# Performance work log

Hardware: AMD Instinct MI355X
Metric: run time of the kernel (lower is better)

## Reference

```python
import jax, jax.numpy as jnp
import numpy as np

B, L, D, H, DF = 8, 1024, 512, 8, 2048
NBLK = 3  # three TemporalAttentionBlocks


def _ln(x, g, b, eps=1e-5):
    m = x.mean(-1, keepdims=True)
    v = x.var(-1, keepdims=True)
    return (x - m) / jnp.sqrt(v + eps) * g + b


def setup_inputs() -> dict:
    key = jax.random.key(0)
    ks = iter(jax.random.split(key, 64))
    def w(i, o):
        return jax.random.normal(next(ks), (i, o), jnp.float32) * (1.0 / np.sqrt(i))
    def ws(n, i, o):
        return jax.random.normal(next(ks), (n, i, o), jnp.float32) * (1.0 / np.sqrt(i))
    return dict(
        x=jax.random.normal(next(ks), (B, L, D), jnp.float32),
        # outer multi-head attention (AttentionLayer) params
        aw_q=w(D, D), ab_q=jnp.zeros((D,), jnp.float32),
        aw_k=w(D, D), ab_k=jnp.zeros((D,), jnp.float32),
        aw_v=w(D, D), ab_v=jnp.zeros((D,), jnp.float32),
        aw_o=w(D, D), ab_o=jnp.zeros((D,), jnp.float32),
        n1g=jnp.ones((D,), jnp.float32), n1b=jnp.zeros((D,), jnp.float32),
        n2g=jnp.ones((D,), jnp.float32), n2b=jnp.zeros((D,), jnp.float32),
        # 3 stacked TemporalAttentionBlock params
        tqw=ws(NBLK, D, D), tqb=jnp.zeros((NBLK, D), jnp.float32),
        tkw=ws(NBLK, D, D), tkb=jnp.zeros((NBLK, D), jnp.float32),
        tvw=ws(NBLK, D, D), tvb=jnp.zeros((NBLK, D), jnp.float32),
        tow=ws(NBLK, D, D), tob=jnp.zeros((NBLK, D), jnp.float32),
        tf1w=ws(NBLK, D, DF), tf1b=jnp.zeros((NBLK, DF), jnp.float32),
        tf2w=ws(NBLK, DF, D), tf2b=jnp.zeros((NBLK, D), jnp.float32),
        tng=jnp.ones((NBLK, D), jnp.float32), tnb=jnp.zeros((NBLK, D), jnp.float32),
    )


def _temporal_block(x, qw, qb, kw, kb, vw, vb, ow, ob, f1w, f1b, f2w, f2b, ng, nb):
    b, l, d = x.shape
    q = x @ qw + qb
    k = x @ kw + kb
    v = x @ vw + vb
    # NOTE: no 1/sqrt(d) scaling, as in the original
    probs = jax.nn.softmax(jnp.einsum('bld,bsd->bls', q, k), axis=-1)
    out = jnp.einsum('bls,bsd->bld', probs, v)
    # faithful to original transpose(1,2).contiguous().view(-1, L, D): a
    # memory-reinterpreting reshape of [B,D,L] into [B,L,D]
    out = jnp.swapaxes(out, 1, 2).reshape(b, l, d)
    x = x + (out @ ow + ob)
    res = x
    xn = _ln(x, ng, nb)
    ff = jax.nn.relu(xn @ f1w + f1b) @ f2w + f2b
    return res + ff


def reference(x, aw_q, ab_q, aw_k, ab_k, aw_v, ab_v, aw_o, ab_o,
              n1g, n1b, n2g, n2b,
              tqw, tqb, tkw, tkb, tvw, tvb, tow, tob,
              tf1w, tf1b, tf2w, tf2b, tng, tnb):
    b, l, d = x.shape
    e = d // H
    q = (x @ aw_q + ab_q).reshape(b, l, H, e)
    k = (x @ aw_k + ab_k).reshape(b, l, H, e)
    v = (x @ aw_v + ab_v).reshape(b, l, H, e)
    A = jax.nn.softmax(jnp.einsum('blhe,bshe->bhls', q, k) / np.sqrt(e).astype(np.float32), axis=-1)
    new_x = jnp.einsum('bhls,bshe->blhe', A, v).reshape(b, l, d) @ aw_o + ab_o
    x = _ln(x + new_x, n1g, n1b)
    y = x
    for i in range(NBLK):
        y = _temporal_block(y, tqw[i], tqb[i], tkw[i], tkb[i], tvw[i], tvb[i],
                            tow[i], tob[i], tf1w[i], tf1b[i], tf2w[i], tf2b[i],
                            tng[i], tnb[i])
    return _ln(x + y, n2g, n2b), A
```

## Files before the change

kernel.cpp:

```cpp
#include <hip/hip_runtime.h>

typedef __bf16 bf16;
typedef __bf16 v8bf __attribute__((ext_vector_type(8)));
typedef float  v4f  __attribute__((ext_vector_type(4)));

#define BM 128
#define BN 128
#define BK 32

enum { EPI_STORE = 0, EPI_RELU = 1, EPI_ADD = 2 };

template <int SPLIT, int EPI, typename CT>
__global__ __launch_bounds__(256)
void gemm_bt(const bf16* __restrict__ A, long plA,
             const bf16* __restrict__ Bt, long plB,
             const float* __restrict__ bias, long sBias,
             const bf16* __restrict__ R, long plR,
             CT* __restrict__ C, long plC,
             int M, int N, int K, int lda, int ldb, int ldc,
             long sA, long sB, long sC, long sR,
             int zdiv, long sA2, long sB2, long sC2,
             float scale)
{
    constexpr int NBUF = SPLIT ? 4 : 2;
    constexpr int TILE = BM * BK;
    __shared__ __attribute__((aligned(16))) bf16 lds[2 * NBUF * TILE];

    const int bz = blockIdx.z;
    const int zq = bz / zdiv;
    const int zr = bz - zq * zdiv;
    A  += (long)zq * sA + (long)zr * sA2;
    Bt += (long)zq * sB + (long)zr * sB2;
    C  += (long)zq * sC + (long)zr * sC2;
    const float* bp = bias ? bias + (long)bz * sBias : nullptr;
    const bf16* Rp = (EPI == EPI_ADD) ? (R + (long)zq * sR) : (const bf16*)nullptr;

    const int tn = blockIdx.x * BN;
    const int tm = blockIdx.y * BM;
    const int tid  = threadIdx.x;
    const int wave = tid >> 6;
    const int lane = tid & 63;
    const int wm   = (wave >> 1) * 64;
    const int wn   = (wave & 1) * 64;
    const int quad = lane >> 4;
    const int l16  = lane & 15;

    v4f acc[4][4];
#pragma unroll
    for (int i = 0; i < 4; ++i)
#pragma unroll
        for (int j = 0; j < 4; ++j) {
            v4f z = {0.f, 0.f, 0.f, 0.f};
            acc[i][j] = z;
        }

    const int sr  = lane >> 2;
    const int scl = (lane & 3) * 8;
    const int nT  = K / BK;

    auto stage = [&](int buf, int k0) {
        bf16* const dst = lds + buf * (NBUF * TILE);
#pragma unroll
        for (int c = 0; c < 2; ++c) {
            const int chunk = wave * 2 + c;
            const int row   = chunk * 16 + sr;
            {
                const bf16* gp = A + (long)(tm + row) * lda + (k0 + scl);
                __builtin_amdgcn_global_load_lds(
                    (const __attribute__((address_space(1))) void*)gp,
                    (__attribute__((address_space(3))) void*)(dst + chunk * 512),
                    16, 0, 0);
                if (SPLIT)
                    __builtin_amdgcn_global_load_lds(
                        (const __attribute__((address_space(1))) void*)(gp + plA),
                        (__attribute__((address_space(3))) void*)(dst + 2 * TILE + chunk * 512),
                        16, 0, 0);
            }
            {
                int gn = tn + row;
                if (gn > N - 1) gn = N - 1;
                const bf16* gp = Bt + (long)gn * ldb + (k0 + scl);
                __builtin_amdgcn_global_load_lds(
                    (const __attribute__((address_space(1))) void*)gp,
                    (__attribute__((address_space(3))) void*)(dst + TILE + chunk * 512),
                    16, 0, 0);
                if (SPLIT)
                    __builtin_amdgcn_global_load_lds(
                        (const __attribute__((address_space(1))) void*)(gp + plB),
                        (__attribute__((address_space(3))) void*)(dst + 3 * TILE + chunk * 512),
                        16, 0, 0);
            }
        }
    };

    stage(0, 0);

    for (int t = 0; t < nT; ++t) {
        const int cur = t & 1;
        if (t + 1 < nT) {
            stage(cur ^ 1, (t + 1) * BK);
            if constexpr (SPLIT != 0)
                asm volatile("s_waitcnt vmcnt(8)" ::: "memory");
            else
                asm volatile("s_waitcnt vmcnt(4)" ::: "memory");
        } else {
            asm volatile("s_waitcnt vmcnt(0)" ::: "memory");
        }
        __builtin_amdgcn_s_barrier();
        asm volatile("" ::: "memory");

        const bf16* const lb  = lds + cur * (NBUF * TILE);
        const bf16* const lAh = lb;
        const bf16* const lBh = lb + TILE;

        v8bf ah[4], bh[4];
#pragma unroll
        for (int i = 0; i < 4; ++i) {
            ah[i] = *(const v8bf*)(lAh + (wm + i * 16 + l16) * 32 + quad * 8);
            bh[i] = *(const v8bf*)(lBh + (wn + i * 16 + l16) * 32 + quad * 8);
        }
#pragma unroll
        for (int i = 0; i < 4; ++i)
#pragma unroll
            for (int j = 0; j < 4; ++j)
                acc[i][j] = __builtin_amdgcn_mfma_f32_16x16x32_bf16(
                    ah[i], bh[j], acc[i][j], 0, 0, 0);
        if (SPLIT) {
            const bf16* const lAl = lb + 2 * TILE;
            const bf16* const lBl = lb + 3 * TILE;
            {
                v8bf bl[4];
#pragma unroll
                for (int j = 0; j < 4; ++j)
                    bl[j] = *(const v8bf*)(lBl + (wn + j * 16 + l16) * 32 + quad * 8);
#pragma unroll
                for (int i = 0; i < 4; ++i)
#pragma unroll
                    for (int j = 0; j < 4; ++j)
                        acc[i][j] = __builtin_amdgcn_mfma_f32_16x16x32_bf16(
                            ah[i], bl[j], acc[i][j], 0, 0, 0);
            }
            {
                v8bf al[4];
#pragma unroll
                for (int i = 0; i < 4; ++i)
                    al[i] = *(const v8bf*)(lAl + (wm + i * 16 + l16) * 32 + quad * 8);
#pragma unroll
                for (int i = 0; i < 4; ++i)
#pragma unroll
                    for (int j = 0; j < 4; ++j)
                        acc[i][j] = __builtin_amdgcn_mfma_f32_16x16x32_bf16(
                            al[i], bh[j], acc[i][j], 0, 0, 0);
            }
        }
        __builtin_amdgcn_s_barrier();
        asm volatile("" ::: "memory");
    }

#pragma unroll
    for (int i = 0; i < 4; ++i) {
        const int r0 = tm + wm + i * 16 + quad * 4;
#pragma unroll
        for (int j = 0; j < 4; ++j) {
            const int col = tn + wn + j * 16 + l16;
            if (col < N) {
                const float bv = bp ? bp[col] : 0.f;
#pragma unroll
                for (int r = 0; r < 4; ++r) {
                    const long off = (long)(r0 + r) * ldc + col;
                    float v = acc[i][j][r] * scale + bv;
                    if (EPI == EPI_RELU) v = v > 0.f ? v : 0.f;
                    if (EPI == EPI_ADD)  v += (float)Rp[off] + (float)Rp[off + plR];
                    if constexpr (sizeof(CT) == 4) {
                        C[off] = (CT)v;
                    } else {
                        const bf16 hi = (bf16)v;
                        C[off]       = hi;
                        C[off + plC] = (bf16)(v - (float)hi);
                    }
                }
            }
        }
    }
}

__global__ void detect_dtype(const void* __restrict__ n1g, int* __restrict__ flag)
{
    if (threadIdx.x == 0 && blockIdx.x == 0)
        *flag = (*(const unsigned*)n1g == 0x3F800000u) ? 1 : 0;
}

__global__ __launch_bounds__(256)
void convert_pairs(const void* __restrict__ src, bf16* __restrict__ dst,
                   long plane, int n, const int* __restrict__ flag)
{
    const bool f32 = (*flag != 0);
    const int base = (blockIdx.x * 256 + threadIdx.x) * 8;
#pragma unroll
    for (int i = 0; i < 8; ++i) {
        const int idx = base + i;
        if (idx < n) {
            const float v = f32 ? ((const float*)src)[idx]
                                : (float)((const bf16*)src)[idx];
            const bf16 hi = (bf16)v;
            dst[idx]         = hi;
            dst[idx + plane] = (bf16)(v - (float)hi);
        }
    }
}

struct Seg { const void* src; float* dst; int n; };
struct SegTab { Seg s[17]; };
__global__ __launch_bounds__(256)
void convert_f32(SegTab tab, const int* __restrict__ flag)
{
    const Seg sg = tab.s[blockIdx.z];
    const bool f32 = (*flag != 0);
    const int idx = blockIdx.x * 256 + threadIdx.x;
    if (idx < sg.n)
        sg.dst[idx] = f32 ? ((const float*)sg.src)[idx]
                          : (float)((const bf16*)sg.src)[idx];
}

__global__ __launch_bounds__(256)
void transpose_split(const void* __restrict__ in, bf16* __restrict__ out,
                     int R, int C, const int* __restrict__ flag)
{
    __shared__ float t[32][33];
    const bool f32 = (*flag != 0);
    const long ib = (long)blockIdx.z * R * C;
    bf16* ob = out + (long)blockIdx.z * 2 * R * C;
    const int c0 = blockIdx.x * 32;
    const int r0 = blockIdx.y * 32;
    const int x  = threadIdx.x & 31;
    const int y4 = threadIdx.x >> 5;
#pragma unroll
    for (int i = 0; i < 4; ++i) {
        const int r = y4 * 4 + i;
        const long gi = ib + (long)(r0 + r) * C + c0 + x;
        t[r][x] = f32 ? ((const float*)in)[gi] : (float)((const bf16*)in)[gi];
    }
    __syncthreads();
#pragma unroll
    for (int i = 0; i < 4; ++i) {
        const int oc = y4 * 4 + i;
        const float w = t[x][oc];
        const bf16 hi = (bf16)w;
        const long oo = (long)(c0 + oc) * R + r0 + x;
        ob[oo]             = hi;
        ob[oo + (long)R * C] = (bf16)(w - (float)hi);
    }
}

__global__ __launch_bounds__(256)
void transpose_pair(const bf16* __restrict__ in, bf16* __restrict__ out,
                    int R, int C, long PL, int NB)
{
    __shared__ bf16 t[32][33];
    const int plane = blockIdx.z / NB;
    const int b     = blockIdx.z % NB;
    const long base = (long)plane * PL + (long)b * R * C;
    const int c0 = blockIdx.x * 32;
    const int r0 = blockIdx.y * 32;
    const int x  = threadIdx.x & 31;
    const int y4 = threadIdx.x >> 5;
#pragma unroll
    for (int i = 0; i < 4; ++i) {
        const int r = y4 * 4 + i;
        t[r][x] = in[base + (long)(r0 + r) * C + c0 + x];
    }
    __syncthreads();
#pragma unroll
    for (int i = 0; i < 4; ++i) {
        const int oc = y4 * 4 + i;
        out[base + (long)(c0 + oc) * R + r0 + x] = t[x][oc];
    }
}

__global__ __launch_bounds__(256)
void softmax_rows(const float* __restrict__ in, bf16* __restrict__ probs,
                  long plP, void* __restrict__ aout, long aoff,
                  const int* __restrict__ flag, int L)
{
    const int row  = blockIdx.x * 4 + (threadIdx.x >> 6);
    const int lane = threadIdx.x & 63;
    const bool f32 = aout && (*flag != 0);
    const float* r = in + (long)row * L;
    const int n = L >> 8;
    float ev[16];
    float mx = -3.4e38f;
    for (int t = 0; t < n; ++t) {
        const float4 xx = *(const float4*)(r + t * 256 + lane * 4);
        ev[4 * t]     = xx.x;
        ev[4 * t + 1] = xx.y;
        ev[4 * t + 2] = xx.z;
        ev[4 * t + 3] = xx.w;
        mx = fmaxf(mx, fmaxf(fmaxf(xx.x, xx.y), fmaxf(xx.z, xx.w)));
    }
    for (int o = 32; o; o >>= 1) mx = fmaxf(mx, __shfl_xor(mx, o));
    float s = 0.f;
    for (int t = 0; t < 4 * n; ++t) { ev[t] = __expf(ev[t] - mx); s += ev[t]; }
    for (int o = 32; o; o >>= 1) s += __shfl_xor(s, o);
    const float inv = 1.f / s;
    bf16* w = probs + (long)row * L;
    for (int t = 0; t < n; ++t) {
        const int idx = t * 256 + lane * 4;
        float p[4];
        union { bf16 b[4]; uint2 u; } uh, ul, ua;
#pragma unroll
        for (int j = 0; j < 4; ++j) {
            p[j] = ev[4 * t + j] * inv;
            const bf16 h = (bf16)p[j];
            uh.b[j] = h;
            ul.b[j] = (bf16)(p[j] - (float)h);
        }
        *(uint2*)(w + idx)       = uh.u;
        *(uint2*)(w + idx + plP) = ul.u;
        if (aout) {
            const long o2 = aoff + (long)row * L + idx;
            if (f32) {
                float4 f; f.x = p[0]; f.y = p[1]; f.z = p[2]; f.w = p[3];
                *(float4*)((float*)aout + o2) = f;
            } else {
#pragma unroll
                for (int j = 0; j < 4; ++j) ua.b[j] = (bf16)p[j];
                *(uint2*)((bf16*)aout + o2) = ua.u;
            }
        }
    }
}

template <bool ADD, bool TO_ANY>
__global__ __launch_bounds__(256)
void ln_rows(const bf16* __restrict__ a, const bf16* __restrict__ b2, long PL,
             const float* __restrict__ g, const float* __restrict__ bb,
             bf16* __restrict__ outp, void* __restrict__ out_any,
             const int* __restrict__ flag)
{
    const int row  = blockIdx.x * 4 + (threadIdx.x >> 6);
    const int lane = threadIdx.x & 63;
    const bool f32 = TO_ANY && (*flag != 0);
    const long base = (long)row * 512;
    float v[8];
    float s = 0.f, s2 = 0.f;
#pragma unroll
    for (int t = 0; t < 4; ++t) {
        const long gi = base + t * 128 + lane * 2;
        union { unsigned u; bf16 b[2]; } hh, ll;
        hh.u = *(const unsigned*)(a + gi);
        ll.u = *(const unsigned*)(a + gi + PL);
        float x0 = (float)hh.b[0] + (float)ll.b[0];
        float x1 = (float)hh.b[1] + (float)ll.b[1];
        if (ADD) {
            union { unsigned u; bf16 b[2]; } h2, l2;
            h2.u = *(const unsigned*)(b2 + gi);
            l2.u = *(const unsigned*)(b2 + gi + PL);
            x0 += (float)h2.b[0] + (float)l2.b[0];
            x1 += (float)h2.b[1] + (float)l2.b[1];
        }
        v[2 * t] = x0; v[2 * t + 1] = x1;
        s += x0 + x1; s2 += x0 * x0 + x1 * x1;
    }
    for (int o = 32; o; o >>= 1) { s += __shfl_xor(s, o); s2 += __shfl_xor(s2, o); }
    const float mean = s * (1.f / 512.f);
    const float var  = s2 * (1.f / 512.f) - mean * mean;
    const float rstd = rsqrtf(var + 1e-5f);
#pragma unroll
    for (int t = 0; t < 4; ++t) {
        const int idx = t * 128 + lane * 2;
        const float o0 = (v[2 * t]     - mean) * rstd * g[idx]     + bb[idx];
        const float o1 = (v[2 * t + 1] - mean) * rstd * g[idx + 1] + bb[idx + 1];
        if (TO_ANY) {
            if (f32) {
                float2 f; f.x = o0; f.y = o1;
                *(float2*)((float*)out_any + base + idx) = f;
            } else {
                union { bf16 b[2]; unsigned u; } ua;
                ua.b[0] = (bf16)o0; ua.b[1] = (bf16)o1;
                *(unsigned*)((bf16*)out_any + base + idx) = ua.u;
            }
        } else {
            union { bf16 b[2]; unsigned u; } uh, ul;
            const bf16 h0 = (bf16)o0, h1 = (bf16)o1;
            uh.b[0] = h0; uh.b[1] = h1;
            ul.b[0] = (bf16)(o0 - (float)h0); ul.b[1] = (bf16)(o1 - (float)h1);
            *(unsigned*)(outp + base + idx)      = uh.u;
            *(unsigned*)(outp + base + idx + PL) = ul.u;
        }
    }
}

extern "C" void kernel_launch(void* const* d_in, const int* in_sizes, int n_in,
                              void* d_out, int out_size, void* d_ws, size_t ws_size,
                              hipStream_t stream)
{
    const int B = 8, L = 1024, D = 512, DF = 2048;
    const long BLD = (long)B * L * D;
    const long PLA = BLD;
    const long PLPF = (long)64 * L * L;
    const long PLF = (long)B * L * DF;
    const long WPL = (long)D * D;
    const long FPL = (long)D * DF;

    char* wsb = (char*)d_ws;
    size_t off = 0;
    auto alloc = [&](size_t bytes) -> void* {
        void* p = wsb + off;
        off = (off + bytes + 255) & ~(size_t)255;
        return p;
    };
    int*   flag  = (int*)alloc(256);
    float* abq_f = (float*)alloc(512 * 4);  float* abk_f = (float*)alloc(512 * 4);
    float* abv_f = (float*)alloc(512 * 4);  float* abo_f = (float*)alloc(512 * 4);
    float* n1g_f = (float*)alloc(512 * 4);  float* n1b_f = (float*)alloc(512 * 4);
    float* n2g_f = (float*)alloc(512 * 4);  float* n2b_f = (float*)alloc(512 * 4);
    float* tqb_f = (float*)alloc(1536 * 4); float* tkb_f = (float*)alloc(1536 * 4);
    float* tvb_f = (float*)alloc(1536 * 4); float* tob_f = (float*)alloc(1536 * 4);
    float* tf1b_f = (float*)alloc(6144 * 4); float* tf2b_f = (float*)alloc(1536 * 4);
    float* tng_f = (float*)alloc(1536 * 4); float* tnb_f = (float*)alloc(1536 * 4);
    bf16* awqT  = (bf16*)alloc((size_t)2 * WPL * 2);
    bf16* awkT  = (bf16*)alloc((size_t)2 * WPL * 2);
    bf16* awvT  = (bf16*)alloc((size_t)2 * WPL * 2);
    bf16* awoT  = (bf16*)alloc((size_t)2 * WPL * 2);
    bf16* tqwT  = (bf16*)alloc((size_t)3 * 2 * WPL * 2);
    bf16* tkwT  = (bf16*)alloc((size_t)3 * 2 * WPL * 2);
    bf16* tvwT  = (bf16*)alloc((size_t)3 * 2 * WPL * 2);
    bf16* towT  = (bf16*)alloc((size_t)3 * 2 * WPL * 2);
    bf16* tf1wT = (bf16*)alloc((size_t)3 * 2 * FPL * 2);
    bf16* tf2wT = (bf16*)alloc((size_t)3 * 2 * FPL * 2);
    bf16* x_s    = (bf16*)alloc((size_t)2 * PLA * 2);
    bf16* q      = (bf16*)alloc((size_t)2 * PLA * 2);
    bf16* k      = (bf16*)alloc((size_t)2 * PLA * 2);
    bf16* v      = (bf16*)alloc((size_t)2 * PLA * 2);
    bf16* vT     = (bf16*)alloc((size_t)2 * PLA * 2);
    bf16* x_attn = (bf16*)alloc((size_t)2 * PLA * 2);
    bf16* res    = (bf16*)alloc((size_t)2 * PLA * 2);
    bf16* probs  = (bf16*)alloc((size_t)2 * PLPF * 2);
    char* big    = (char*)alloc(sizeof(float) * (size_t)PLPF);
    float* logits = (float*)big;
    bf16*  ffh    = (bf16*)big;
    bf16* atmp = v;
    bf16* t_re = q;
    bf16* xn   = k;
    bf16* ybuf = x_s;

    const dim3 blk(256);

    detect_dtype<<<dim3(1), dim3(64), 0, stream>>>(d_in[9], flag);
    SegTab tab;
    tab.s[0]  = { d_in[2],  abq_f,  512 };  tab.s[1]  = { d_in[4],  abk_f,  512 };
    tab.s[2]  = { d_in[6],  abv_f,  512 };  tab.s[3]  = { d_in[8],  abo_f,  512 };
    tab.s[4]  = { d_in[9],  n1g_f,  512 };  tab.s[5]  = { d_in[10], n1b_f,  512 };
    tab.s[6]  = { d_in[11], n2g_f,  512 };  tab.s[7]  = { d_in[12], n2b_f,  512 };
    tab.s[8]  = { d_in[14], tqb_f,  1536 }; tab.s[9]  = { d_in[16], tkb_f,  1536 };
    tab.s[10] = { d_in[18], tvb_f,  1536 }; tab.s[11] = { d_in[20], tob_f,  1536 };
    tab.s[12] = { d_in[22], tf1b_f, 6144 }; tab.s[13] = { d_in[24], tf2b_f, 1536 };
    tab.s[14] = { d_in[25], tng_f,  1536 }; tab.s[15] = { d_in[26], tnb_f,  1536 };
    tab.s[16] = { d_in[26], tnb_f,  1536 };
    convert_f32<<<dim3(24, 1, 17), blk, 0, stream>>>(tab, flag);
    convert_pairs<<<dim3(2048), blk, 0, stream>>>(d_in[0], x_s, PLA, (int)BLD, flag);

    transpose_split<<<dim3(16, 16, 1), blk, 0, stream>>>(d_in[1], awqT, D, D, flag);
    transpose_split<<<dim3(16, 16, 1), blk, 0, stream>>>(d_in[3], awkT, D, D, flag);
    transpose_split<<<dim3(16, 16, 1), blk, 0, stream>>>(d_in[5], awvT, D, D, flag);
    transpose_split<<<dim3(16, 16, 1), blk, 0, stream>>>(d_in[7], awoT, D, D, flag);
    transpose_split<<<dim3(16, 16, 3), blk, 0, stream>>>(d_in[13], tqwT, D, D, flag);
    transpose_split<<<dim3(16, 16, 3), blk, 0, stream>>>(d_in[15], tkwT, D, D, flag);
    transpose_split<<<dim3(16, 16, 3), blk, 0, stream>>>(d_in[17], tvwT, D, D, flag);
    transpose_split<<<dim3(16, 16, 3), blk, 0, stream>>>(d_in[19], towT, D, D, flag);
    transpose_split<<<dim3(64, 16, 3), blk, 0, stream>>>(d_in[21], tf1wT, D, DF, flag);
    transpose_split<<<dim3(16, 64, 3), blk, 0, stream>>>(d_in[23], tf2wT, DF, D, flag);

    gemm_bt<1, EPI_STORE, bf16><<<dim3(4, 64, 3), blk, 0, stream>>>(
        x_s, PLA, awqT, WPL, abq_f, 512, nullptr, 0, q, PLA,
        8192, 512, 512, 512, 512, 512,
        0, (long)2 * WPL, (long)2 * PLA, 0, 1, 0, 0, 0, 1.f);
    transpose_pair<<<dim3(16, 32, 16), blk, 0, stream>>>(v, vT, L, D, PLA, 8);

    gemm_bt<1, EPI_STORE, float><<<dim3(8, 8, 64), blk, 0, stream>>>(
        q, PLA, k, PLA, nullptr, 0, nullptr, 0, logits, 0,
        1024, 1024, 64, 512, 512, 1024,
        (long)L * D, (long)L * D, (long)8 * L * L, 0,
        8, 64, 64, (long)L * L, 0.125f);
    softmax_rows<<<dim3(16384), blk, 0, stream>>>(
        logits, probs, PLPF, d_out, BLD, flag, L);
    gemm_bt<1, EPI_STORE, bf16><<<dim3(1, 8, 64), blk, 0, stream>>>(
        probs, PLPF, vT, PLA, nullptr, 0, nullptr, 0, atmp, PLA,
        1024, 64, 1024, 1024, 1024, 512,
        (long)8 * L * L, (long)D * L, (long)L * D, 0,
        8, (long)L * L, (long)64 * L, 64, 1.f);

    gemm_bt<1, EPI_ADD, bf16><<<dim3(4, 64, 1), blk, 0, stream>>>(
        atmp, PLA, awoT, WPL, abo_f, 0, x_s, PLA, res, PLA,
        8192, 512, 512, 512, 512, 512, 0, 0, 0, 0, 1, 0, 0, 0, 1.f);
    ln_rows<false, false><<<dim3(2048), blk, 0, stream>>>(
        res, nullptr, PLA, n1g_f, n1b_f, x_attn, nullptr, flag);

    const bf16* yin = x_attn;
    for (int t = 0; t < 3; ++t) {
        const bf16* owT = towT + (long)t * 2 * WPL;
        const bf16* f1T = tf1wT + (long)t * 2 * FPL;
        const bf16* f2T = tf2wT + (long)t * 2 * FPL;

        gemm_bt<1, EPI_STORE, bf16><<<dim3(4, 64, 3), blk, 0, stream>>>(
            yin, PLA, tqwT + (long)t * 2 * WPL, WPL, tqb_f + t * D, 1536,
            nullptr, 0, q, PLA,
            8192, 512, 512, 512, 512, 512,
            0, (long)6 * WPL, (long)2 * PLA, 0, 1, 0, 0, 0, 1.f);
        transpose_pair<<<dim3(16, 32, 16), blk, 0, stream>>>(v, vT, L, D, PLA, 8);

        gemm_bt<1, EPI_STORE, float><<<dim3(8, 8, 8), blk, 0, stream>>>(
            q, PLA, k, PLA, nullptr, 0, nullptr, 0, logits, 0,
            1024, 1024, 512, 512, 512, 1024,
            (long)L * D, (long)L * D, (long)L * L, 0, 1, 0, 0, 0, 1.f);
        softmax_rows<<<dim3(2048), blk, 0, stream>>>(
            logits, probs, PLPF, nullptr, 0, flag, L);
        gemm_bt<1, EPI_STORE, bf16><<<dim3(4, 8, 8), blk, 0, stream>>>(
            probs, PLPF, vT, PLA, nullptr, 0, nullptr, 0, atmp, PLA,
            1024, 512, 1024, 1024, 1024, 512,
            (long)L * L, (long)D * L, (long)L * D, 0, 1, 0, 0, 0, 1.f);
        transpose_pair<<<dim3(16, 32, 16), blk, 0, stream>>>(atmp, t_re, L, D, PLA, 8);
        gemm_bt<1, EPI_ADD, bf16><<<dim3(4, 64, 1), blk, 0, stream>>>(
            t_re, PLA, owT, WPL, tob_f + t * D, 0, yin, PLA, res, PLA,
            8192, 512, 512, 512, 512, 512, 0, 0, 0, 0, 1, 0, 0, 0, 1.f);
        ln_rows<false, false><<<dim3(2048), blk, 0, stream>>>(
            res, nullptr, PLA, tng_f + t * D, tnb_f + t * D, xn, nullptr, flag);
        gemm_bt<1, EPI_RELU, bf16><<<dim3(16, 64, 1), blk, 0, stream>>>(
            xn, PLA, f1T, FPL, tf1b_f + t * DF, 0, nullptr, 0, ffh, PLF,
            8192, 2048, 512, 512, 512, 2048, 0, 0, 0, 0, 1, 0, 0, 0, 1.f);
        gemm_bt<1, EPI_ADD, bf16><<<dim3(4, 64, 1), blk, 0, stream>>>(
            ffh, PLF, f2T, FPL, tf2b_f + t * D, 0, res, PLA, ybuf, PLA,
            8192, 512, 2048, 2048, 2048, 512, 0, 0, 0, 0, 1, 0, 0, 0, 1.f);
        yin = ybuf;
    }

    ln_rows<true, true><<<dim3(2048), blk, 0, stream>>>(
        x_attn, ybuf, PLA, n2g_f, n2b_f, nullptr, d_out, flag);
}
```

Before: 1.816 ms.

## Template GEMM on N-tile and pipeline depth; vectorize transpose, convert and layernorm

Result: no change. 1.790 ms (-1.4%).

```diff
diff --git a/kernel.cpp b/kernel.cpp
--- a/kernel.cpp
+++ b/kernel.cpp
@@ -5,12 +5,13 @@
 typedef float  v4f  __attribute__((ext_vector_type(4)));
 
 #define BM 128
-#define BN 128
 #define BK 32
 
 enum { EPI_STORE = 0, EPI_RELU = 1, EPI_ADD = 2 };
 
-template <int SPLIT, int EPI, typename CT>
+#define WAITN(n) asm volatile("s_waitcnt vmcnt(" #n ")" ::: "memory")
+
+template <int SPLIT, int EPI, typename CT, int NT, int DEPTH>
 __global__ __launch_bounds__(256)
 void gemm_bt(const bf16* __restrict__ A, long plA,
              const bf16* __restrict__ Bt, long plB,
@@ -22,9 +23,18 @@
              int zdiv, long sA2, long sB2, long sC2,
              float scale)
 {
-    constexpr int NBUF = SPLIT ? 4 : 2;
-    constexpr int TILE = BM * BK;
-    __shared__ __attribute__((aligned(16))) bf16 lds[2 * NBUF * TILE];
+    constexpr int TILE_A = BM * BK;
+    constexpr int TILE_B = NT * BK;
+    constexpr int OFF_AH = 0;
+    constexpr int OFF_BH = TILE_A;
+    constexpr int OFF_AL = TILE_A + TILE_B;
+    constexpr int OFF_BL = 2 * TILE_A + TILE_B;
+    constexpr int SETSZ  = (SPLIT ? 2 : 1) * (TILE_A + TILE_B);
+    constexpr bool N64   = (NT == 64);
+    constexpr int  WR    = N64 ? 2 : 4;
+    constexpr int LPT = (SPLIT ? 2 : 1) * (2 + (N64 ? 1 : 2));
+
+    __shared__ __attribute__((aligned(16))) bf16 lds[DEPTH * SETSZ];
 
     const int bz = blockIdx.z;
     const int zq = bz / zdiv;
@@ -35,19 +45,19 @@
     const float* bp = bias ? bias + (long)bz * sBias : nullptr;
     const bf16* Rp = (EPI == EPI_ADD) ? (R + (long)zq * sR) : (const bf16*)nullptr;
 
-    const int tn = blockIdx.x * BN;
+    const int tn = blockIdx.x * NT;
     const int tm = blockIdx.y * BM;
     const int tid  = threadIdx.x;
     const int wave = tid >> 6;
     const int lane = tid & 63;
-    const int wm   = (wave >> 1) * 64;
-    const int wn   = (wave & 1) * 64;
+    const int wm   = N64 ? wave * 32 : (wave >> 1) * 64;
+    const int wn   = N64 ? 0 : (wave & 1) * 64;
     const int quad = lane >> 4;
     const int l16  = lane & 15;
 
-    v4f acc[4][4];
-#pragma unroll
-    for (int i = 0; i < 4; ++i)
+    v4f acc[WR][4];
+#pragma unroll
+    for (int i = 0; i < WR; ++i)
 #pragma unroll
         for (int j = 0; j < 4; ++j) {
             v4f z = {0.f, 0.f, 0.f, 0.f};
@@ -59,94 +69,108 @@
     const int nT  = K / BK;
 
     auto stage = [&](int buf, int k0) {
-        bf16* const dst = lds + buf * (NBUF * TILE);
+        bf16* const dst = lds + buf * SETSZ;
 #pragma unroll
         for (int c = 0; c < 2; ++c) {
-            const int chunk = wave * 2 + c;
-            const int row   = chunk * 16 + sr;
             {
+                const int chunk = wave * 2 + c;
+                const int row   = chunk * 16 + sr;
                 const bf16* gp = A + (long)(tm + row) * lda + (k0 + scl);
                 __builtin_amdgcn_global_load_lds(
                     (const __attribute__((address_space(1))) void*)gp,
-                    (__attribute__((address_space(3))) void*)(dst + chunk * 512),
+                    (__attribute__((address_space(3))) void*)(dst + OFF_AH + chunk * 512),
                     16, 0, 0);
                 if (SPLIT)
                     __builtin_amdgcn_global_load_lds(
                         (const __attribute__((address_space(1))) void*)(gp + plA),
-                        (__attribute__((address_space(3))) void*)(dst + 2 * TILE + chunk * 512),
+                        (__attribute__((address_space(3))) void*)(dst + OFF_AL + chunk * 512),
                         16, 0, 0);
             }
-            {
+            if (!N64 || c == 0) {
+                const int chunk = N64 ? wave : wave * 2 + c;
+                const int row   = chunk * 16 + sr;
                 int gn = tn + row;
                 if (gn > N - 1) gn = N - 1;
                 const bf16* gp = Bt + (long)gn * ldb + (k0 + scl);
                 __builtin_amdgcn_global_load_lds(
                     (const __attribute__((address_space(1))) void*)gp,
-                    (__attribute__((address_space(3))) void*)(dst + TILE + chunk * 512),
+                    (__attribute__((address_space(3))) void*)(dst + OFF_BH + chunk * 512),
                     16, 0, 0);
                 if (SPLIT)
                     __builtin_amdgcn_global_load_lds(
                         (const __attribute__((address_space(1))) void*)(gp + plB),
-                        (__attribute__((address_space(3))) void*)(dst + 3 * TILE + chunk * 512),
+                        (__attribute__((address_space(3))) void*)(dst + OFF_BL + chunk * 512),
                         16, 0, 0);
             }
         }
     };
 
     stage(0, 0);
-
+    if (DEPTH == 3 && nT > 1) stage(1, BK);
+
+    int cur = 0;
     for (int t = 0; t < nT; ++t) {
-        const int cur = t & 1;
-        if (t + 1 < nT) {
-            stage(cur ^ 1, (t + 1) * BK);
-            if constexpr (SPLIT != 0)
-                asm volatile("s_waitcnt vmcnt(8)" ::: "memory");
-            else
-                asm volatile("s_waitcnt vmcnt(4)" ::: "memory");
+        const int pbuf = (cur == 0) ? (DEPTH - 1) : (cur - 1);
+        if (t + DEPTH - 1 < nT)
+            stage(pbuf, (t + DEPTH - 1) * BK);
+
+        const int infl0 = nT - 1 - t;
+        const int infl = infl0 < DEPTH - 1 ? infl0 : DEPTH - 1;
+        if (infl == 2) {
+            if constexpr (LPT == 8) WAITN(16);
+            else if constexpr (LPT == 6) WAITN(12);
+            else if constexpr (LPT == 4) WAITN(8);
+            else WAITN(6);
+        } else if (infl == 1) {
+            if constexpr (LPT == 8) WAITN(8);
+            else if constexpr (LPT == 6) WAITN(6);
+            else if constexpr (LPT == 4) WAITN(4);
+            else WAITN(3);
         } else {
-            asm volatile("s_waitcnt vmcnt(0)" ::: "memory");
+            WAITN(0);
         }
         __builtin_amdgcn_s_barrier();
         asm volatile("" ::: "memory");
 
-        const bf16* const lb  = lds + cur * (NBUF * TILE);
-        const bf16* const lAh = lb;
-        const bf16* const lBh = lb + TILE;
-
-        v8bf ah[4], bh[4];
-#pragma unroll
-        for (int i = 0; i < 4; ++i) {
+        const bf16* const lb  = lds + cur * SETSZ;
+        const bf16* const lAh = lb + OFF_AH;
+        const bf16* const lBh = lb + OFF_BH;
+
+        v8bf ah[WR], bh[4];
+#pragma unroll
+        for (int i = 0; i < WR; ++i)
             ah[i] = *(const v8bf*)(lAh + (wm + i * 16 + l16) * 32 + quad * 8);
-            bh[i] = *(const v8bf*)(lBh + (wn + i * 16 + l16) * 32 + quad * 8);
-        }
-#pragma unroll
-        for (int i = 0; i < 4; ++i)
+#pragma unroll
+        for (int j = 0; j < 4; ++j)
+            bh[j] = *(const v8bf*)(lBh + (wn + j * 16 + l16) * 32 + quad * 8);
+#pragma unroll
+        for (int i = 0; i < WR; ++i)
 #pragma unroll
             for (int j = 0; j < 4; ++j)
                 acc[i][j] = __builtin_amdgcn_mfma_f32_16x16x32_bf16(
                     ah[i], bh[j], acc[i][j], 0, 0, 0);
         if (SPLIT) {
-            const bf16* const lAl = lb + 2 * TILE;
-            const bf16* const lBl = lb + 3 * TILE;
+            const bf16* const lAl = lb + OFF_AL;
+            const bf16* const lBl = lb + OFF_BL;
             {
                 v8bf bl[4];
 #pragma unroll
                 for (int j = 0; j < 4; ++j)
                     bl[j] = *(const v8bf*)(lBl + (wn + j * 16 + l16) * 32 + quad * 8);
 #pragma unroll
-                for (int i = 0; i < 4; ++i)
+                for (int i = 0; i < WR; ++i)
 #pragma unroll
                     for (int j = 0; j < 4; ++j)
                         acc[i][j] = __builtin_amdgcn_mfma_f32_16x16x32_bf16(
                             ah[i], bl[j], acc[i][j], 0, 0, 0);
             }
             {
-                v8bf al[4];
-#pragma unroll
-                for (int i = 0; i < 4; ++i)
+                v8bf al[WR];
+#pragma unroll
+                for (int i = 0; i < WR; ++i)
                     al[i] = *(const v8bf*)(lAl + (wm + i * 16 + l16) * 32 + quad * 8);
 #pragma unroll
-                for (int i = 0; i < 4; ++i)
+                for (int i = 0; i < WR; ++i)
 #pragma unroll
                     for (int j = 0; j < 4; ++j)
                         acc[i][j] = __builtin_amdgcn_mfma_f32_16x16x32_bf16(
@@ -155,10 +179,11 @@
         }
         __builtin_amdgcn_s_barrier();
         asm volatile("" ::: "memory");
-    }
-
-#pragma unroll
-    for (int i = 0; i < 4; ++i) {
+        cur = (cur + 1 == DEPTH) ? 0 : cur + 1;
+    }
+
+#pragma unroll
+    for (int i = 0; i < WR; ++i) {
         const int r0 = tm + wm + i * 16 + quad * 4;
 #pragma unroll
         for (int j = 0; j < 4; ++j) {
@@ -196,17 +221,40 @@
 {
     const bool f32 = (*flag != 0);
     const int base = (blockIdx.x * 256 + threadIdx.x) * 8;
+    if (base + 7 >= n) {
+        for (int i = 0; i < 8; ++i) {
+            const int idx = base + i;
+            if (idx < n) {
+                const float v = f32 ? ((const float*)src)[idx]
+                                    : (float)((const bf16*)src)[idx];
+                const bf16 hi = (bf16)v;
+                dst[idx]         = hi;
+                dst[idx + plane] = (bf16)(v - (float)hi);
+            }
+        }
+        return;
+    }
+    float v[8];
+    if (f32) {
+        const float4 a = *(const float4*)((const float*)src + base);
+        const float4 b = *(const float4*)((const float*)src + base + 4);
+        v[0]=a.x; v[1]=a.y; v[2]=a.z; v[3]=a.w;
+        v[4]=b.x; v[5]=b.y; v[6]=b.z; v[7]=b.w;
+    } else {
+        union { uint4 u; bf16 b[8]; } s;
+        s.u = *(const uint4*)((const bf16*)src + base);
+#pragma unroll
+        for (int i = 0; i < 8; ++i) v[i] = (float)s.b[i];
+    }
+    union { bf16 b[8]; uint4 u; } hi, lo;
 #pragma unroll
     for (int i = 0; i < 8; ++i) {
-        const int idx = base + i;
-        if (idx < n) {
-            const float v = f32 ? ((const float*)src)[idx]
-                                : (float)((const bf16*)src)[idx];
-            const bf16 hi = (bf16)v;
-            dst[idx]         = hi;
-            dst[idx + plane] = (bf16)(v - (float)hi);
-        }
-    }
+        const bf16 h = (bf16)v[i];
+        hi.b[i] = h;
+        lo.b[i] = (bf16)(v[i] - (float)h);
+    }
+    *(uint4*)(dst + base)         = hi.u;
+    *(uint4*)(dst + base + plane) = lo.u;
 }
 
 struct Seg { const void* src; float* dst; int n; };
@@ -256,24 +304,30 @@
 void transpose_pair(const bf16* __restrict__ in, bf16* __restrict__ out,
                     int R, int C, long PL, int NB)
 {
-    __shared__ bf16 t[32][33];
+    __shared__ unsigned short t[64][72];
     const int plane = blockIdx.z / NB;
     const int b     = blockIdx.z % NB;
     const long base = (long)plane * PL + (long)b * R * C;
-    const int c0 = blockIdx.x * 32;
-    const int r0 = blockIdx.y * 32;
-    const int x  = threadIdx.x & 31;
-    const int y4 = threadIdx.x >> 5;
-#pragma unroll
-    for (int i = 0; i < 4; ++i) {
-        const int r = y4 * 4 + i;
-        t[r][x] = in[base + (long)(r0 + r) * C + c0 + x];
+    const int c0 = blockIdx.x * 64;
+    const int r0 = blockIdx.y * 64;
+    const int x  = threadIdx.x & 15;
+    const int y  = threadIdx.x >> 4;
+#pragma unroll
+    for (int p = 0; p < 4; ++p) {
+        const int row = y + p * 16;
+        const ushort4 v = *(const ushort4*)((const unsigned short*)in
+                          + base + (long)(r0 + row) * C + c0 + x * 4);
+        t[x * 4 + 0][row] = v.x;
+        t[x * 4 + 1][row] = v.y;
+        t[x * 4 + 2][row] = v.z;
+        t[x * 4 + 3][row] = v.w;
     }
     __syncthreads();
 #pragma unroll
-    for (int i = 0; i < 4; ++i) {
-        const int oc = y4 * 4 + i;
-        out[base + (long)(c0 + oc) * R + r0 + x] = t[x][oc];
+    for (int p = 0; p < 4; ++p) {
+        const int oc = y + p * 16;
+        const ushort4 v = *(const ushort4*)(&t[oc][x * 4]);
+        *(ushort4*)((unsigned short*)out + base + (long)(c0 + oc) * R + r0 + x * 4) = v;
     }
 }
 
@@ -344,48 +398,61 @@
     float v[8];
     float s = 0.f, s2 = 0.f;
 #pragma unroll
-    for (int t = 0; t < 4; ++t) {
-        const long gi = base + t * 128 + lane * 2;
-        union { unsigned u; bf16 b[2]; } hh, ll;
-        hh.u = *(const unsigned*)(a + gi);
-        ll.u = *(const unsigned*)(a + gi + PL);
-        float x0 = (float)hh.b[0] + (float)ll.b[0];
-        float x1 = (float)hh.b[1] + (float)ll.b[1];
+    for (int t = 0; t < 2; ++t) {
+        const long gi = base + t * 256 + lane * 4;
+        union { uint2 u; bf16 b[4]; } hh, ll;
+        hh.u = *(const uint2*)(a + gi);
+        ll.u = *(const uint2*)(a + gi + PL);
+        float x[4];
+#pragma unroll
+        for (int j = 0; j < 4; ++j) x[j] = (float)hh.b[j] + (float)ll.b[j];
         if (ADD) {
-            union { unsigned u; bf16 b[2]; } h2, l2;
-            h2.u = *(const unsigned*)(b2 + gi);
-            l2.u = *(const unsigned*)(b2 + gi + PL);
-            x0 += (float)h2.b[0] + (float)l2.b[0];
-            x1 += (float)h2.b[1] + (float)l2.b[1];
-        }
-        v[2 * t] = x0; v[2 * t + 1] = x1;
-        s += x0 + x1; s2 += x0 * x0 + x1 * x1;
+            union { uint2 u; bf16 b[4]; } h2, l2;
+            h2.u = *(const uint2*)(b2 + gi);
+            l2.u = *(const uint2*)(b2 + gi + PL);
+#pragma unroll
+            for (int j = 0; j < 4; ++j) x[j] += (float)h2.b[j] + (float)l2.b[j];
+        }
+#pragma unroll
+        for (int j = 0; j < 4; ++j) {
+            v[4 * t + j] = x[j];
+            s += x[j]; s2 += x[j] * x[j];
+        }
     }
     for (int o = 32; o; o >>= 1) { s += __shfl_xor(s, o); s2 += __shfl_xor(s2, o); }
     const float mean = s * (1.f / 512.f);
     const float var  = s2 * (1.f / 512.f) - mean * mean;
     const float rstd = rsqrtf(var + 1e-5f);
 #pragma unroll
-    for (int t = 0; t < 4; ++t) {
-        const int idx = t * 128 + lane * 2;
-        const float o0 = (v[2 * t]     - mean) * rstd * g[idx]     + bb[idx];
-        const float o1 = (v[2 * t + 1] - mean) * rstd * g[idx + 1] + bb[idx + 1];
+    for (int t = 0; t < 2; ++t) {
+        const int idx = t * 256 + lane * 4;
+        const float4 gg = *(const float4*)(g + idx);
+        const float4 bbv = *(const float4*)(bb + idx);
+        float o[4];
+        o[0] = (v[4*t]   - mean) * rstd * gg.x + bbv.x;
+        o[1] = (v[4*t+1] - mean) * rstd * gg.y + bbv.y;
+        o[2] = (v[4*t+2] - mean) * rstd * gg.z + bbv.z;
+        o[3] = (v[4*t+3] - mean) * rstd * gg.w + bbv.w;
         if (TO_ANY) {
             if (f32) {
-                float2 f; f.x = o0; f.y = o1;
-                *(float2*)((float*)out_any + base + idx) = f;
+                float4 f; f.x = o[0]; f.y = o[1]; f.z = o[2]; f.w = o[3];
+                *(float4*)((float*)out_any + base + idx) = f;
             } else {
-                union { bf16 b[2]; unsigned u; } ua;
-                ua.b[0] = (bf16)o0; ua.b[1] = (bf16)o1;
-                *(unsigned*)((bf16*)out_any + base + idx) = ua.u;
+                union { bf16 b[4]; uint2 u; } ua;
+#pragma unroll
+                for (int j = 0; j < 4; ++j) ua.b[j] = (bf16)o[j];
+                *(uint2*)((bf16*)out_any + base + idx) = ua.u;
             }
         } else {
-            union { bf16 b[2]; unsigned u; } uh, ul;
-            const bf16 h0 = (bf16)o0, h1 = (bf16)o1;
-            uh.b[0] = h0; uh.b[1] = h1;
-            ul.b[0] = (bf16)(o0 - (float)h0); ul.b[1] = (bf16)(o1 - (float)h1);
-            *(unsigned*)(outp + base + idx)      = uh.u;
-            *(unsigned*)(outp + base + idx + PL) = ul.u;
+            union { bf16 b[4]; uint2 u; } uh, ul;
+#pragma unroll
+            for (int j = 0; j < 4; ++j) {
+                const bf16 h = (bf16)o[j];
+                uh.b[j] = h;
+                ul.b[j] = (bf16)(o[j] - (float)h);
+            }
+            *(uint2*)(outp + base + idx)      = uh.u;
+            *(uint2*)(outp + base + idx + PL) = ul.u;
         }
     }
 }
@@ -471,26 +538,26 @@
     transpose_split<<<dim3(64, 16, 3), blk, 0, stream>>>(d_in[21], tf1wT, D, DF, flag);
     transpose_split<<<dim3(16, 64, 3), blk, 0, stream>>>(d_in[23], tf2wT, DF, D, flag);
 
-    gemm_bt<1, EPI_STORE, bf16><<<dim3(4, 64, 3), blk, 0, stream>>>(
+    gemm_bt<1, EPI_STORE, bf16, 128, 2><<<dim3(4, 64, 3), blk, 0, stream>>>(
         x_s, PLA, awqT, WPL, abq_f, 512, nullptr, 0, q, PLA,
         8192, 512, 512, 512, 512, 512,
         0, (long)2 * WPL, (long)2 * PLA, 0, 1, 0, 0, 0, 1.f);
-    transpose_pair<<<dim3(16, 32, 16), blk, 0, stream>>>(v, vT, L, D, PLA, 8);
-
-    gemm_bt<1, EPI_STORE, float><<<dim3(8, 8, 64), blk, 0, stream>>>(
+    transpose_pair<<<dim3(8, 16, 16), blk, 0, stream>>>(v, vT, L, D, PLA, 8);
+
+    gemm_bt<1, EPI_STORE, float, 128, 2><<<dim3(8, 8, 64), blk, 0, stream>>>(
         q, PLA, k, PLA, nullptr, 0, nullptr, 0, logits, 0,
         1024, 1024, 64, 512, 512, 1024,
         (long)L * D, (long)L * D, (long)8 * L * L, 0,
         8, 64, 64, (long)L * L, 0.125f);
     softmax_rows<<<dim3(16384), blk, 0, stream>>>(
         logits, probs, PLPF, d_out, BLD, flag, L);
-    gemm_bt<1, EPI_STORE, bf16><<<dim3(1, 8, 64), blk, 0, stream>>>(
+    gemm_bt<1, EPI_STORE, bf16, 64, 2><<<dim3(1, 8, 64), blk, 0, stream>>>(
         probs, PLPF, vT, PLA, nullptr, 0, nullptr, 0, atmp, PLA,
         1024, 64, 1024, 1024, 1024, 512,
         (long)8 * L * L, (long)D * L, (long)L * D, 0,
         8, (long)L * L, (long)64 * L, 64, 1.f);
 
-    gemm_bt<1, EPI_ADD, bf16><<<dim3(4, 64, 1), blk, 0, stream>>>(
+    gemm_bt<1, EPI_ADD, bf16, 128, 3><<<dim3(4, 64, 1), blk, 0, stream>>>(
         atmp, PLA, awoT, WPL, abo_f, 0, x_s, PLA, res, PLA,
         8192, 512, 512, 512, 512, 512, 0, 0, 0, 0, 1, 0, 0, 0, 1.f);
     ln_rows<false, false><<<dim3(2048), blk, 0, stream>>>(
@@ -502,33 +569,33 @@
         const bf16* f1T = tf1wT + (long)t * 2 * FPL;
         const bf16* f2T = tf2wT + (long)t * 2 * FPL;
 
-        gemm_bt<1, EPI_STORE, bf16><<<dim3(4, 64, 3), blk, 0, stream>>>(
+        gemm_bt<1, EPI_STORE, bf16, 128, 2><<<dim3(4, 64, 3), blk, 0, stream>>>(
             yin, PLA, tqwT + (long)t * 2 * WPL, WPL, tqb_f + t * D, 1536,
             nullptr, 0, q, PLA,
             8192, 512, 512, 512, 512, 512,
             0, (long)6 * WPL, (long)2 * PLA, 0, 1, 0, 0, 0, 1.f);
-        transpose_pair<<<dim3(16, 32, 16), blk, 0, stream>>>(v, vT, L, D, PLA, 8);
-
-        gemm_bt<1, EPI_STORE, float><<<dim3(8, 8, 8), blk, 0, stream>>>(
+        transpose_pair<<<dim3(8, 16, 16), blk, 0, stream>>>(v, vT, L, D, PLA, 8);
+
+        gemm_bt<1, EPI_STORE, float, 128, 2><<<dim3(8, 8, 8), blk, 0, stream>>>(
             q, PLA, k, PLA, nullptr, 0, nullptr, 0, logits, 0,
             1024, 1024, 512, 512, 512, 1024,
             (long)L * D, (long)L * D, (long)L * L, 0, 1, 0, 0, 0, 1.f);
         softmax_rows<<<dim3(2048), blk, 0, stream>>>(
             logits, probs, PLPF, nullptr, 0, flag, L);
-        gemm_bt<1, EPI_STORE, bf16><<<dim3(4, 8, 8), blk, 0, stream>>>(
+        gemm_bt<1, EPI_STORE, bf16, 128, 3><<<dim3(4, 8, 8), blk, 0, stream>>>(
             probs, PLPF, vT, PLA, nullptr, 0, nullptr, 0, atmp, PLA,
             1024, 512, 1024, 1024, 1024, 512,
             (long)L * L, (long)D * L, (long)L * D, 0, 1, 0, 0, 0, 1.f);
-        transpose_pair<<<dim3(16, 32, 16), blk, 0, stream>>>(atmp, t_re, L, D, PLA, 8);
-        gemm_bt<1, EPI_ADD, bf16><<<dim3(4, 64, 1), blk, 0, stream>>>(
+        transpose_pair<<<dim3(8, 16, 16), blk, 0, stream>>>(atmp, t_re, L, D, PLA, 8);
+        gemm_bt<1, EPI_ADD, bf16, 128, 3><<<dim3(4, 64, 1), blk, 0, stream>>>(
             t_re, PLA, owT, WPL, tob_f + t * D, 0, yin, PLA, res, PLA,
             8192, 512, 512, 512, 512, 512, 0, 0, 0, 0, 1, 0, 0, 0, 1.f);
         ln_rows<false, false><<<dim3(2048), blk, 0, stream>>>(
             res, nullptr, PLA, tng_f + t * D, tnb_f + t * D, xn, nullptr, flag);
-        gemm_bt<1, EPI_RELU, bf16><<<dim3(16, 64, 1), blk, 0, stream>>>(
+        gemm_bt<1, EPI_RELU, bf16, 128, 2><<<dim3(16, 64, 1), blk, 0, stream>>>(
             xn, PLA, f1T, FPL, tf1b_f + t * DF, 0, nullptr, 0, ffh, PLF,
             8192, 2048, 512, 512, 512, 2048, 0, 0, 0, 0, 1, 0, 0, 0, 1.f);
-        gemm_bt<1, EPI_ADD, bf16><<<dim3(4, 64, 1), blk, 0, stream>>>(
+        gemm_bt<1, EPI_ADD, bf16, 128, 3><<<dim3(4, 64, 1), blk, 0, stream>>>(
             ffh, PLF, f2T, FPL, tf2b_f + t * D, 0, res, PLA, ybuf, PLA,
             8192, 512, 2048, 2048, 2048, 512, 0, 0, 0, 0, 1, 0, 0, 0, 1.f);
         yin = ybuf;
```
